# Kernel tuning notes

Measured on AMD Instinct MI355X. Metric: run time of the kernel, lower is better.

## Reference

```python
import jax, jax.numpy as jnp
import numpy as np

B, S, D, H = 4, 2048, 1024, 16
HD = D // H  # head_dim = 64
SCALE = HD ** -0.5


def setup_inputs() -> dict:
    key = jax.random.key(0)
    k1, k2, k3, k4, k5 = jax.random.split(key, 5)
    std = D ** -0.5
    return {
        "x": jax.random.normal(k1, (B, S, D), dtype=jnp.float32),
        "w_qkv": jax.random.normal(k2, (D, 3 * D), dtype=jnp.float32) * std,
        "b_qkv": jax.random.normal(k3, (3 * D,), dtype=jnp.float32) * 0.01,
        "w_out": jax.random.normal(k4, (D, D), dtype=jnp.float32) * std,
        "b_out": jax.random.normal(k5, (D,), dtype=jnp.float32) * 0.01,
    }


def reference(x, w_qkv, b_qkv, w_out, b_out):
    b, s, d = x.shape
    qkv = x @ w_qkv + b_qkv                                   # [B,S,3D]
    qkv = qkv.reshape(b, s, 3, H, HD).transpose(2, 0, 3, 1, 4)  # [3,B,H,S,HD]
    q, k, v = qkv[0], qkv[1], qkv[2]
    attn = jnp.einsum("bhqd,bhkd->bhqk", q, k) * SCALE        # [B,H,S,S]
    attn = jax.nn.softmax(attn, axis=-1)
    out = jnp.einsum("bhqk,bhkd->bhqd", attn, v)              # [B,H,S,HD]
    out = out.transpose(0, 2, 1, 3).reshape(b, s, d)          # [B,S,D]
    return out @ w_out + b_out
```

## Files before the change

kernel.cpp:

```cpp
#include <hip/hip_runtime.h>
#include <stdint.h>
#include <stddef.h>

#define NB 4
#define NS 2048
#define ND 1024
#define NH 16
#define HDIM 64
#define SCALE 0.125f
#define CLOG2E 0.18033688011112042f

typedef __attribute__((ext_vector_type(4))) float f32x4;
typedef __attribute__((ext_vector_type(16))) float f32x16;
typedef __attribute__((ext_vector_type(8))) __bf16 bf16x8;
typedef __attribute__((ext_vector_type(4))) uint32_t u32x4;

__device__ __forceinline__ uint16_t f2bf(float f) {
  uint32_t u = __builtin_bit_cast(uint32_t, f);
  return (uint16_t)((u + 0x7fffu + ((u >> 16) & 1u)) >> 16);
}

__device__ __forceinline__ void gload_lds16(const void* g, void* l) {
  __builtin_amdgcn_global_load_lds((const __attribute__((address_space(1))) void*)g,
                                   (__attribute__((address_space(3))) void*)l, 16, 0, 0);
}

__device__ __forceinline__ uint32_t cvtpk(float lo, float hi) {
  uint32_t r;
  asm("v_cvt_pk_bf16_f32 %0, %1, %2" : "=v"(r) : "v"(lo), "v"(hi));
  return r;
}

__device__ __forceinline__ void permswap(uint32_t& a, uint32_t& b) {
  asm("v_permlane32_swap_b32 %0, %1" : "+v"(a), "+v"(b));
}

__device__ __forceinline__ float fexp2(float x) {
  float r;
  asm("v_exp_f32 %0, %1" : "=v"(r) : "v"(x));
  return r;
}

__global__ __launch_bounds__(256)
void k_prep(const float* __restrict__ x, const float* __restrict__ wq,
            const float* __restrict__ wo, uint16_t* __restrict__ Xb,
            uint16_t* __restrict__ Wq, uint16_t* __restrict__ Wo) {
  __shared__ float tile[64][65];
  const int bid = blockIdx.x, tid = threadIdx.x;
  if (bid < 8192) {
    int i = bid * 256 + tid;
    float4 v = reinterpret_cast<const float4*>(x)[i];
    ushort4 o;
    o.x = f2bf(v.x); o.y = f2bf(v.y); o.z = f2bf(v.z); o.w = f2bf(v.w);
    reinterpret_cast<ushort4*>(Xb)[i] = o;
    return;
  }
  const float* in; uint16_t* out; int K, N, bx, by;
  if (bid < 8960) { int r = bid - 8192; in = wq; out = Wq; K = 1024; N = 3072; bx = r % 48; by = r / 48; }
  else            { int r = bid - 8960; in = wo; out = Wo; K = 1024; N = 1024; bx = r % 16; by = r / 16; }
  const int nb = bx * 64, kb = by * 64;
  const int c = tid & 63, r0 = tid >> 6;
#pragma unroll
  for (int i = 0; i < 16; ++i) {
    int r = r0 * 16 + i;
    tile[r][c] = in[(size_t)(kb + r) * N + nb + c];
  }
  __syncthreads();
#pragma unroll
  for (int i = 0; i < 16; ++i) {
    int rr = r0 * 16 + i;
    out[(size_t)(nb + rr) * K + kb + c] = f2bf(tile[c][rr]);
  }
}

__global__ __launch_bounds__(512)
void k_gemm256(const uint16_t* __restrict__ A, const uint16_t* __restrict__ Bt,
               const float* __restrict__ bias, uint16_t* __restrict__ C,
               uint16_t* __restrict__ vt, int M, int N, int K) {
  __shared__ __align__(16) char Al[2][32768];
  __shared__ __align__(16) char Bl[2][32768];
  const int tid = threadIdx.x, wave = tid >> 6, lane = tid & 63;

  const int flat = blockIdx.y * gridDim.x + blockIdx.x;
  const int cpx = (gridDim.x * gridDim.y) >> 3;
  const int swz = (flat & 7) * cpx + (flat >> 3);
  const int bx = swz % gridDim.x, by = swz / gridDim.x;
  const int mb = by * 256, nb = bx * 256;

  const int wm = wave >> 2, wn = wave & 3;
  const int fr = lane & 15, cc = lane >> 4;
  f32x4 acc[8][4] = {};
  const int NT = K >> 6;
  const int sslot = tid & 7;

#define STAGE(BUF, KT) do {                                                     \
    const int kb_ = (KT) * 64;                                                  \
    _Pragma("unroll")                                                           \
    for (int i = 0; i < 4; ++i) {                                               \
      int row = (i * 512 + tid) >> 3;                                           \
      int ch = sslot ^ (row & 7);                                               \
      gload_lds16(A + (size_t)(mb + row) * K + kb_ + ch * 8,                    \
                  Al[BUF] + (size_t)(i * 512 + (wave << 6)) * 16);              \
    }                                                                           \
    _Pragma("unroll")                                                           \
    for (int i = 0; i < 4; ++i) {                                               \
      int row = (i * 512 + tid) >> 3;                                           \
      int ch = sslot ^ (row & 7);                                               \
      gload_lds16(Bt + (size_t)(nb + row) * K + kb_ + ch * 8,                   \
                  Bl[BUF] + (size_t)(i * 512 + (wave << 6)) * 16);              \
    }                                                                           \
  } while (0)

  STAGE(0, 0);
  asm volatile("s_waitcnt vmcnt(0)" ::: "memory");
  __builtin_amdgcn_s_barrier();

  for (int kt = 0; kt < NT; ++kt) {
    const int cur = kt & 1;
    const bool issue = (kt + 1 < NT);
    if (issue) STAGE(cur ^ 1, kt + 1);

#pragma unroll
    for (int ks = 0; ks < 2; ++ks) {
      bf16x8 af[8], bfg[4];
#pragma unroll
      for (int i = 0; i < 8; ++i) {
        int ra = wm * 128 + i * 16 + fr;
        af[i] = *(const bf16x8*)(Al[cur] + ra * 128 + (((ks * 4 + cc) ^ (ra & 7)) * 16));
      }
#pragma unroll
      for (int j = 0; j < 4; ++j) {
        int rb = wn * 64 + j * 16 + fr;
        bfg[j] = *(const bf16x8*)(Bl[cur] + rb * 128 + (((ks * 4 + cc) ^ (rb & 7)) * 16));
      }
      __builtin_amdgcn_s_setprio(1);
#pragma unroll
      for (int i = 0; i < 8; ++i)
#pragma unroll
        for (int j = 0; j < 4; ++j)
          acc[i][j] = __builtin_amdgcn_mfma_f32_16x16x32_bf16(af[i], bfg[j], acc[i][j], 0, 0, 0);
      __builtin_amdgcn_s_setprio(0);
    }

    if (issue) {
      asm volatile("s_waitcnt vmcnt(0)" ::: "memory");
      __builtin_amdgcn_s_barrier();
    }
  }
#undef STAGE

  if (nb < 2048) {
    const float qs = (nb < 1024) ? CLOG2E : 1.0f;
#pragma unroll
    for (int i = 0; i < 8; ++i)
#pragma unroll
      for (int j = 0; j < 4; ++j)
#pragma unroll
        for (int r = 0; r < 4; ++r) {
          int row = mb + wm * 128 + i * 16 + cc * 4 + r;
          int col = nb + wn * 64 + j * 16 + fr;
          C[(size_t)row * N + col] = f2bf((acc[i][j][r] + bias[col]) * qs);
        }
  } else {
    const int b_ = mb >> 11;
    const int h_ = ((nb - 2048) >> 6) + wn;
    const int s0 = (mb & 2047) + wm * 128;
    uint16_t* vb = vt + (size_t)(b_ * 16 + h_) * 64 * NS;
#pragma unroll
    for (int i = 0; i < 8; ++i)
#pragma unroll
      for (int j = 0; j < 4; ++j) {
        int col = nb + wn * 64 + j * 16 + fr;
        int d = j * 16 + fr;
        float bcol = bias[col];
        ushort4 o;
        o.x = f2bf(acc[i][j][0] + bcol);
        o.y = f2bf(acc[i][j][1] + bcol);
        o.z = f2bf(acc[i][j][2] + bcol);
        o.w = f2bf(acc[i][j][3] + bcol);
        int s = s0 + i * 16 + cc * 4;
        *reinterpret_cast<ushort4*>(vb + (size_t)d * NS + s) = o;
      }
  }
}

template<int OUT_BF16>
__global__ __launch_bounds__(256)
void k_gemm(const uint16_t* __restrict__ A, const uint16_t* __restrict__ Bt,
            const float* __restrict__ bias, void* __restrict__ C,
            int M, int N, int K) {
  __shared__ __align__(16) char Al[8192];
  __shared__ __align__(16) char Bl[8192];
  const int tid = threadIdx.x;
  const int wave = tid >> 6, lane = tid & 63;
  const int mb = blockIdx.y * 128, nb = blockIdx.x * 128;
  const int wm = (wave >> 1) * 64, wn = (wave & 1) * 64;
  const int fr = lane & 15, cc = lane >> 4;
  const int srow = tid >> 2, sch = tid & 3;
  f32x4 acc[4][4] = {};

  for (int kb = 0; kb < K; kb += 32) {
#pragma unroll
    for (int p = 0; p < 2; ++p) {
      int row = p * 64 + srow;
      int cg = sch ^ (row & 3) ^ ((row >> 2) & 3);
      gload_lds16(A + (size_t)(mb + row) * K + kb + cg * 8, Al + p * 4096 + wave * 1024);
      gload_lds16(Bt + (size_t)(nb + row) * K + kb + cg * 8, Bl + p * 4096 + wave * 1024);
    }
    __syncthreads();
    bf16x8 af[4], bfr[4];
#pragma unroll
    for (int i = 0; i < 4; ++i) {
      int ra = wm + i * 16 + fr;
      af[i] = *(const bf16x8*)(Al + ra * 64 + ((cc ^ (ra & 3) ^ ((ra >> 2) & 3)) * 16));
      int rb = wn + i * 16 + fr;
      bfr[i] = *(const bf16x8*)(Bl + rb * 64 + ((cc ^ (rb & 3) ^ ((rb >> 2) & 3)) * 16));
    }
#pragma unroll
    for (int i = 0; i < 4; ++i)
#pragma unroll
      for (int j = 0; j < 4; ++j)
        acc[i][j] = __builtin_amdgcn_mfma_f32_16x16x32_bf16(af[i], bfr[j], acc[i][j], 0, 0, 0);
    __syncthreads();
  }

#pragma unroll
  for (int i = 0; i < 4; ++i)
#pragma unroll
    for (int j = 0; j < 4; ++j)
#pragma unroll
      for (int r = 0; r < 4; ++r) {
        int row = mb + wm + i * 16 + cc * 4 + r;
        int col = nb + wn + j * 16 + fr;
        float v = acc[i][j][r] + bias[col];
        if (OUT_BF16)
          ((uint16_t*)C)[(size_t)row * N + col] = f2bf(v);
        else
          ((float*)C)[(size_t)row * N + col] = v;
      }
}

__global__ __launch_bounds__(256)
void k_attn(const uint16_t* __restrict__ qkv, const uint16_t* __restrict__ vt,
            uint16_t* __restrict__ out, int bh0) {
  __shared__ __align__(16) char Kl[2][8192];
  __shared__ __align__(16) char Vl[2][8192];

  const int id = blockIdx.y * 16 + blockIdx.x;
  const int wfid = (id & 7) * 64 + (id >> 3);
  const int bh = bh0 + (wfid >> 4), qblk = wfid & 15;
  const int b = bh >> 4, h = bh & 15;
  const int tid = threadIdx.x, wave = tid >> 6, lane = tid & 63;
  const int ln31 = lane & 31, hi = lane >> 5;

  const int q0 = qblk * 128 + wave * 32;
  const uint16_t* qrowp = qkv + (size_t)(b * NS + q0 + ln31) * 3072 + h * 64 + hi * 8;
  bf16x8 qf[4];
#pragma unroll
  for (int kk = 0; kk < 4; ++kk) qf[kk] = *(const bf16x8*)(qrowp + kk * 16);

  const int srow = tid >> 3;
  const int cs = (tid & 7) ^ (srow & 7);
  const uint16_t* ksrc = qkv + (size_t)(b * NS) * 3072 + 1024 + h * 64 + cs * 8;
  const uint16_t* vsrc = vt + (size_t)bh * 64 * NS + cs * 8;

  f32x16 acc0 = {}, acc1 = {};
  float l_run = 0.f;

#pragma unroll
  for (int r = 0; r < 2; ++r) {
    int row = srow + r * 32;
    gload_lds16(ksrc + (size_t)row * 3072, Kl[0] + wave * 1024 + r * 4096);
    gload_lds16(vsrc + (size_t)row * NS, Vl[0] + wave * 1024 + r * 4096);
  }
  __syncthreads();

  const int ksw = ln31 & 7;

  for (int t = 0; t < NS / 64; ++t) {
    const int cur = t & 1;
    if (t < NS / 64 - 1) {
      const int kb2 = (t + 1) * 64;
      char* kd = Kl[cur ^ 1] + wave * 1024;
      char* vd = Vl[cur ^ 1] + wave * 1024;
#pragma unroll
      for (int r = 0; r < 2; ++r) {
        int row = srow + r * 32;
        gload_lds16(ksrc + (size_t)(kb2 + row) * 3072, kd + r * 4096);
        gload_lds16(vsrc + (size_t)row * NS + kb2, vd + r * 4096);
      }
    }

    const char* kb0 = Kl[cur] + ln31 * 128;
    const char* kb1 = kb0 + 32 * 128;
    f32x16 st0 = {}, st1 = {};
    __builtin_amdgcn_s_setprio(1);
#pragma unroll
    for (int kk = 0; kk < 4; ++kk) {
      int c = ((kk * 2 + hi) ^ ksw) * 16;
      bf16x8 k0 = *(const bf16x8*)(kb0 + c);
      bf16x8 k1 = *(const bf16x8*)(kb1 + c);
      st0 = __builtin_amdgcn_mfma_f32_32x32x16_bf16(k0, qf[kk], st0, 0, 0, 0);
      st1 = __builtin_amdgcn_mfma_f32_32x32x16_bf16(k1, qf[kk], st1, 0, 0, 0);
    }
    __builtin_amdgcn_s_setprio(0);

    float rs = 0.f;
#pragma unroll
    for (int r = 0; r < 16; ++r) { st0[r] = fexp2(st0[r]); rs += st0[r]; }
#pragma unroll
    for (int r = 0; r < 16; ++r) { st1[r] = fexp2(st1[r]); rs += st1[r]; }
    l_run += rs;

    const char* vb0 = Vl[cur] + ln31 * 128;
    const char* vb1 = vb0 + 32 * 128;
    __builtin_amdgcn_s_setprio(1);
#pragma unroll
    for (int h2 = 0; h2 < 2; ++h2) {
      f32x16 ph = h2 ? st1 : st0;
#pragma unroll
      for (int s2 = 0; s2 < 2; ++s2) {
        const int kkp = h2 * 2 + s2;
        const int s8 = s2 * 8;
        uint32_t A0 = cvtpk(ph[s8 + 0], ph[s8 + 1]);
        uint32_t A1 = cvtpk(ph[s8 + 2], ph[s8 + 3]);
        uint32_t B0 = cvtpk(ph[s8 + 4], ph[s8 + 5]);
        uint32_t B1 = cvtpk(ph[s8 + 6], ph[s8 + 7]);
        permswap(A0, B0);
        permswap(A1, B1);
        u32x4 pw = {A0, A1, B0, B1};
        bf16x8 pf = __builtin_bit_cast(bf16x8, pw);
        int c = ((kkp * 2 + hi) ^ ksw) * 16;
        bf16x8 v0 = *(const bf16x8*)(vb0 + c);
        bf16x8 v1 = *(const bf16x8*)(vb1 + c);
        acc0 = __builtin_amdgcn_mfma_f32_32x32x16_bf16(v0, pf, acc0, 0, 0, 0);
        acc1 = __builtin_amdgcn_mfma_f32_32x32x16_bf16(v1, pf, acc1, 0, 0, 0);
      }
    }
    __builtin_amdgcn_s_setprio(0);

    __syncthreads();
  }

  const float rl = 1.0f / (l_run + __shfl_xor(l_run, 32));
  char* sc = (char*)Kl + wave * 4096 + ln31 * 128;
  const int qsw = ln31 & 15;
#pragma unroll
  for (int dn = 0; dn < 2; ++dn) {
    f32x16 a = dn ? acc1 : acc0;
#pragma unroll
    for (int g = 0; g < 4; ++g) {
      uint2 w;
      w.x = cvtpk(a[4 * g + 0] * rl, a[4 * g + 1] * rl);
      w.y = cvtpk(a[4 * g + 2] * rl, a[4 * g + 3] * rl);
      int c8 = (dn * 8 + 2 * g + hi) ^ qsw;
      *(uint2*)(sc + c8 * 8) = w;
    }
  }
  char* outp = (char*)out + ((size_t)(b * NS + q0 + ln31) * 1024 + h * 64 + hi * 32) * 2;
#pragma unroll
  for (int cc2 = 0; cc2 < 4; ++cc2) {
    uint2 va = *(const uint2*)(sc + (((hi * 8 + 2 * cc2 + 0) ^ qsw) * 8));
    uint2 vb2 = *(const uint2*)(sc + (((hi * 8 + 2 * cc2 + 1) ^ qsw) * 8));
    u32x4 o = {va.x, va.y, vb2.x, vb2.y};
    *(u32x4*)(outp + cc2 * 16) = o;
  }
}

extern "C" void kernel_launch(void* const* d_in, const int* in_sizes, int n_in,
                              void* d_out, int out_size, void* d_ws, size_t ws_size,
                              hipStream_t stream) {
  const float* x     = (const float*)d_in[0];
  const float* w_qkv = (const float*)d_in[1];
  const float* b_qkv = (const float*)d_in[2];
  const float* w_out = (const float*)d_in[3];
  const float* b_out = (const float*)d_in[4];
  float* out = (float*)d_out;
  char* ws = (char*)d_ws;

  uint16_t* Xb    = (uint16_t*)(ws);
  uint16_t* Wqkvt = (uint16_t*)(ws + (16u << 20));
  uint16_t* Woutt = (uint16_t*)(ws + (22u << 20));
  uint16_t* QKV   = (uint16_t*)(ws + (24u << 20));
  uint16_t* Vt    = (uint16_t*)(ws + (72u << 20));
  uint16_t* AO    = Xb;

  k_prep<<<9216, 256, 0, stream>>>(x, w_qkv, w_out, Xb, Wqkvt, Woutt);
  k_gemm256<<<dim3(12, 32), 512, 0, stream>>>(Xb, Wqkvt, b_qkv, QKV, Vt, NB * NS, 3 * ND, ND);
  k_attn<<<dim3(16, 32), 256, 0, stream>>>(QKV, Vt, AO, 0);
  k_attn<<<dim3(16, 32), 256, 0, stream>>>(QKV, Vt, AO, 32);
  k_gemm<0><<<dim3(8, 64), 256, 0, stream>>>(AO, Woutt, b_out, out, NB * NS, ND, ND);
}
```

Baseline: 211.0 us.

## Split GEMM k-tile into half stages with interleaved loads and MFMA phases

Restructures the 256x256 GEMM main loop so each 64-wide k-tile is split into two 32-wide halves with separate LDS buffers. Global-to-LDS loads for the next tile are issued in small chunks between four MFMA phases, using partial vmcnt waits and barriers, instead of one bulk stage followed by a full wait. The intent is finer-grained overlap of memory traffic with matrix math and lower fragment register pressure, since only 4 A fragments are held at a time. The cost is many more workgroup barriers per iteration and tricky wait-count correctness.

```diff
diff --git a/kernel.cpp b/kernel.cpp
--- a/kernel.cpp
+++ b/kernel.cpp
@@ -77,8 +77,8 @@
 void k_gemm256(const uint16_t* __restrict__ A, const uint16_t* __restrict__ Bt,
                const float* __restrict__ bias, uint16_t* __restrict__ C,
                uint16_t* __restrict__ vt, int M, int N, int K) {
-  __shared__ __align__(16) char Al[2][32768];
-  __shared__ __align__(16) char Bl[2][32768];
+  __shared__ __align__(16) char Al[2][2][16384];
+  __shared__ __align__(16) char Bl[2][2][16384];
   const int tid = threadIdx.x, wave = tid >> 6, lane = tid & 63;
 
   const int flat = blockIdx.y * gridDim.x + blockIdx.x;
@@ -91,63 +91,90 @@
   const int fr = lane & 15, cc = lane >> 4;
   f32x4 acc[8][4] = {};
   const int NT = K >> 6;
-  const int sslot = tid & 7;
-
-#define STAGE(BUF, KT) do {                                                     \
-    const int kb_ = (KT) * 64;                                                  \
-    _Pragma("unroll")                                                           \
-    for (int i = 0; i < 4; ++i) {                                               \
-      int row = (i * 512 + tid) >> 3;                                           \
-      int ch = sslot ^ (row & 7);                                               \
-      gload_lds16(A + (size_t)(mb + row) * K + kb_ + ch * 8,                    \
-                  Al[BUF] + (size_t)(i * 512 + (wave << 6)) * 16);              \
-    }                                                                           \
-    _Pragma("unroll")                                                           \
-    for (int i = 0; i < 4; ++i) {                                               \
-      int row = (i * 512 + tid) >> 3;                                           \
-      int ch = sslot ^ (row & 7);                                               \
-      gload_lds16(Bt + (size_t)(nb + row) * K + kb_ + ch * 8,                   \
-                  Bl[BUF] + (size_t)(i * 512 + (wave << 6)) * 16);              \
-    }                                                                           \
+
+  const int srow0 = tid >> 2;
+  const int ch0 = (tid & 3) ^ (srow0 & 3);
+  const int dst0 = wave << 10;
+
+#define STGA(BUF, KH, KT) do {                                                   \
+    const uint16_t* g_ = A + (size_t)(mb + srow0) * K + (KT) * 64 + (KH) * 32 + ch0 * 8; \
+    char* d_ = (char*)Al + ((BUF) * 2 + (KH)) * 16384 + dst0;                    \
+    gload_lds16(g_, d_);                                                         \
+    gload_lds16(g_ + (size_t)128 * K, d_ + 8192);                                \
   } while (0)
-
-  STAGE(0, 0);
-  asm volatile("s_waitcnt vmcnt(0)" ::: "memory");
+#define STGB(BUF, KH, KT) do {                                                   \
+    const uint16_t* g_ = Bt + (size_t)(nb + srow0) * K + (KT) * 64 + (KH) * 32 + ch0 * 8; \
+    char* d_ = (char*)Bl + ((BUF) * 2 + (KH)) * 16384 + dst0;                    \
+    gload_lds16(g_, d_);                                                         \
+    gload_lds16(g_ + (size_t)128 * K, d_ + 8192);                                \
+  } while (0)
+#define RDA(I0, KH) do {                                                         \
+    _Pragma("unroll")                                                            \
+    for (int i_ = 0; i_ < 4; ++i_) {                                             \
+      int ra = wm * 128 + ((I0) + i_) * 16 + fr;                                 \
+      af[i_] = *(const bf16x8*)((char*)Al + (cur * 2 + (KH)) * 16384 + ra * 64 + ((cc ^ (ra & 3)) * 16)); \
+    }                                                                            \
+  } while (0)
+#define RDB(KH) do {                                                             \
+    _Pragma("unroll")                                                            \
+    for (int j_ = 0; j_ < 4; ++j_) {                                             \
+      int rb = wn * 64 + j_ * 16 + fr;                                           \
+      bfg[j_] = *(const bf16x8*)((char*)Bl + (cur * 2 + (KH)) * 16384 + rb * 64 + ((cc ^ (rb & 3)) * 16)); \
+    }                                                                            \
+  } while (0)
+#define MM(I0) do {                                                              \
+    __builtin_amdgcn_s_setprio(1);                                               \
+    _Pragma("unroll")                                                            \
+    for (int i_ = 0; i_ < 4; ++i_)                                               \
+      _Pragma("unroll")                                                          \
+      for (int j_ = 0; j_ < 4; ++j_)                                             \
+        acc[(I0) + i_][j_] = __builtin_amdgcn_mfma_f32_16x16x32_bf16(af[i_], bfg[j_], acc[(I0) + i_][j_], 0, 0, 0); \
+    __builtin_amdgcn_s_setprio(0);                                               \
+  } while (0)
+
+  STGA(0, 0, 0); STGB(0, 0, 0); STGA(0, 1, 0); STGB(0, 1, 0);
+  asm volatile("s_waitcnt vmcnt(4)" ::: "memory");
   __builtin_amdgcn_s_barrier();
+  __builtin_amdgcn_sched_barrier(0);
 
   for (int kt = 0; kt < NT; ++kt) {
     const int cur = kt & 1;
-    const bool issue = (kt + 1 < NT);
-    if (issue) STAGE(cur ^ 1, kt + 1);
-
-#pragma unroll
-    for (int ks = 0; ks < 2; ++ks) {
-      bf16x8 af[8], bfg[4];
-#pragma unroll
-      for (int i = 0; i < 8; ++i) {
-        int ra = wm * 128 + i * 16 + fr;
-        af[i] = *(const bf16x8*)(Al[cur] + ra * 128 + (((ks * 4 + cc) ^ (ra & 7)) * 16));
-      }
-#pragma unroll
-      for (int j = 0; j < 4; ++j) {
-        int rb = wn * 64 + j * 16 + fr;
-        bfg[j] = *(const bf16x8*)(Bl[cur] + rb * 128 + (((ks * 4 + cc) ^ (rb & 7)) * 16));
-      }
-      __builtin_amdgcn_s_setprio(1);
-#pragma unroll
-      for (int i = 0; i < 8; ++i)
-#pragma unroll
-        for (int j = 0; j < 4; ++j)
-          acc[i][j] = __builtin_amdgcn_mfma_f32_16x16x32_bf16(af[i], bfg[j], acc[i][j], 0, 0, 0);
-      __builtin_amdgcn_s_setprio(0);
-    }
-
-    if (issue) {
-      asm volatile("s_waitcnt vmcnt(0)" ::: "memory");
-      __builtin_amdgcn_s_barrier();
-    }
-  }
-#undef STAGE
+    const bool st = (kt + 1 < NT);
+    bf16x8 af[4], bfg[4];
+
+    RDA(0, 0); RDB(0);
+    if (st) STGA(cur ^ 1, 0, kt + 1);
+    __builtin_amdgcn_s_barrier();
+    MM(0);
+    __builtin_amdgcn_s_barrier();
+
+    RDA(4, 0);
+    if (st) { STGB(cur ^ 1, 0, kt + 1); asm volatile("s_waitcnt vmcnt(4)" ::: "memory"); }
+    else    { asm volatile("s_waitcnt vmcnt(0)" ::: "memory"); }
+    __builtin_amdgcn_s_barrier();
+    __builtin_amdgcn_sched_barrier(0);
+    MM(4);
+    __builtin_amdgcn_s_barrier();
+
+    RDA(0, 1); RDB(1);
+    if (st) STGA(cur ^ 1, 1, kt + 1);
+    __builtin_amdgcn_s_barrier();
+    MM(0);
+    __builtin_amdgcn_s_barrier();
+
+    RDA(4, 1);
+    if (st) { STGB(cur ^ 1, 1, kt + 1); asm volatile("s_waitcnt vmcnt(4)" ::: "memory"); }
+    else    { asm volatile("s_waitcnt vmcnt(0)" ::: "memory"); }
+    __builtin_amdgcn_s_barrier();
+    __builtin_amdgcn_sched_barrier(0);
+    MM(4);
+    __builtin_amdgcn_s_barrier();
+  }
+#undef MM
+#undef RDB
+#undef RDA
+#undef STGB
+#undef STGA
 
   if (nb < 2048) {
     const float qs = (nb < 1024) ? CLOG2E : 1.0f;
```

Result: no change. 211.2 us (+0.1%).
